# Kernel tuning notes

Measured on AMD Instinct MI355X. Metric: run time of the kernel, lower is better.

## Reference

```python
import jax, jax.numpy as jnp
import numpy as np

SCALE_POS = 2.0
SCALE_NEG = 40.0
THRESH_POS = 0.5
THRESH_NEG = 0.5
MARGIN = 0.1
EPS = 1e-5


def setup_inputs() -> dict:
    key = jax.random.key(0)
    kf, kl = jax.random.split(key)
    B, D, NUM_CLASSES = 4096, 1024, 64
    feats = jax.random.normal(kf, (B, D), dtype=jnp.float32)
    feats = feats / jnp.linalg.norm(feats, axis=1, keepdims=True)  # L2-normalized embeddings
    labels = jax.random.randint(kl, (B,), 0, NUM_CLASSES, dtype=jnp.int64)
    return {"feats": feats, "labels": labels}


def reference(feats, labels):
    B = feats.shape[0]
    sim = jnp.matmul(feats, feats.T)  # [B, B]
    same = labels[:, None] == labels[None, :]
    pos_mask = same & (sim < 1.0 - EPS)  # drop self / near-duplicate pairs
    neg_mask = ~same

    # hard mining: keep negatives above min positive - margin, positives below max negative + margin
    min_pos = jnp.min(jnp.where(pos_mask, sim, jnp.inf), axis=1)   # [B]
    max_neg = jnp.max(jnp.where(neg_mask, sim, -jnp.inf), axis=1)  # [B]
    neg_sel = neg_mask & (sim + MARGIN > min_pos[:, None])
    pos_sel = pos_mask & (sim - MARGIN < max_neg[:, None])

    pos_sum = jnp.sum(jnp.where(pos_sel, jnp.exp(-SCALE_POS * (sim - THRESH_POS)), 0.0), axis=1)
    neg_sum = jnp.sum(jnp.where(neg_sel, jnp.exp(SCALE_NEG * (sim - THRESH_NEG)), 0.0), axis=1)
    pos_loss = jnp.log1p(pos_sum) / SCALE_POS
    neg_loss = jnp.log1p(neg_sum) / SCALE_NEG

    valid = jnp.any(pos_sel, axis=1) & jnp.any(neg_sel, axis=1)  # rows skipped by original loop
    return jnp.sum(jnp.where(valid, pos_loss + neg_loss, 0.0)) / B
```

## Files before the change

kernel.cpp:

```cpp
#include <hip/hip_runtime.h>

typedef float floatx4 __attribute__((ext_vector_type(4)));
typedef int intx4 __attribute__((ext_vector_type(4)));
typedef int intx8 __attribute__((ext_vector_type(8)));
typedef __attribute__((address_space(1))) const void gvoid;
typedef __attribute__((address_space(3))) void svoid;

#define SCALE_POS 2.0f
#define SCALE_NEG 40.0f
#define THRESH 0.5f
#define MARGIN 0.1f
#define EPSV 1e-5f

__global__ void k_init(const float* __restrict__ feats,
                       unsigned char* __restrict__ f8,
                       float* __restrict__ out,
                       int total4) {
    int i = blockIdx.x * blockDim.x + threadIdx.x;
    if (i < total4) {
        float4 v = ((const float4*)feats)[i];
        int w = 0;
        w = __builtin_amdgcn_cvt_pk_fp8_f32(v.x, v.y, w, false);
        w = __builtin_amdgcn_cvt_pk_fp8_f32(v.z, v.w, w, true);
        ((int*)f8)[i] = w;
    }
    if (i == 0) out[0] = 0.f;
}

__global__ void __launch_bounds__(256, 4)
k_gemmA(const unsigned char* __restrict__ f8,
        const int* __restrict__ labels,
        float* __restrict__ pmin,
        float* __restrict__ pmax,
        int D, int nb) {
    __shared__ __align__(16) unsigned char As[128 * 128];
    __shared__ __align__(16) unsigned char Bs[128 * 128];
    __shared__ int labR[128], labC[128];

    const int bid0 = blockIdx.x;
    const int t = (bid0 & 7) * 66 + (bid0 >> 3);
    int rb = 0, rem = t;
    while (rem >= nb - rb) { rem -= nb - rb; ++rb; }
    const int cb = rb + rem;
    const int rowBase = rb * 128;
    const int colBase = cb * 128;

    const int tid = threadIdx.x;
    const int lane = tid & 63;
    const int wave = tid >> 6;
    const int wr = wave >> 1;
    const int wc = wave & 1;
    const int q = lane >> 4;
    const int cIn = lane & 15;

    if (tid < 128) labR[tid] = labels[rowBase + tid];
    else           labC[tid - 128] = labels[colBase + (tid - 128)];

    const int subrow = lane >> 3;
    const int swz = (lane & 7) ^ subrow;
    const unsigned char* gP[8];
    unsigned char* lP[8];
#pragma unroll
    for (int j = 0; j < 8; ++j) {
        const int c = wave * 8 + j;
        const int grow = (c < 16) ? (rowBase + c * 8 + subrow)
                                  : (colBase + (c - 16) * 8 + subrow);
        gP[j] = f8 + (size_t)grow * D + swz * 16;
        lP[j] = ((c < 16) ? (As + c * 1024) : (Bs + (c - 16) * 1024)) + lane * 16;
    }

    int aOff0[4], aOff1[4], bOff0[4], bOff1[4];
#pragma unroll
    for (int i = 0; i < 4; ++i) {
        const int rA = wr * 64 + i * 16 + cIn;
        aOff0[i] = rA * 128 + ((2 * q) ^ (rA & 7)) * 16;
        aOff1[i] = rA * 128 + ((2 * q + 1) ^ (rA & 7)) * 16;
        const int rB = wc * 64 + i * 16 + cIn;
        bOff0[i] = rB * 128 + ((2 * q) ^ (rB & 7)) * 16;
        bOff1[i] = rB * 128 + ((2 * q + 1) ^ (rB & 7)) * 16;
    }

    floatx4 acc[4][4] = {};

    const int KT = D >> 7;
    for (int kt = 0; kt < KT; ++kt) {
        const int kOff = kt * 128;
        __syncthreads();
#pragma unroll
        for (int j = 0; j < 8; ++j)
            __builtin_amdgcn_global_load_lds((gvoid*)(gP[j] + kOff), (svoid*)lP[j], 16, 0, 0);
        __syncthreads();

        intx8 a[4], b[4];
#pragma unroll
        for (int i = 0; i < 4; ++i) {
            intx4 lo = *(const intx4*)(As + aOff0[i]);
            intx4 hi = *(const intx4*)(As + aOff1[i]);
            a[i] = __builtin_shufflevector(lo, hi, 0, 1, 2, 3, 4, 5, 6, 7);
        }
#pragma unroll
        for (int i = 0; i < 4; ++i) {
            intx4 lo = *(const intx4*)(Bs + bOff0[i]);
            intx4 hi = *(const intx4*)(Bs + bOff1[i]);
            b[i] = __builtin_shufflevector(lo, hi, 0, 1, 2, 3, 4, 5, 6, 7);
        }
#pragma unroll
        for (int i = 0; i < 4; ++i)
#pragma unroll
            for (int j2 = 0; j2 < 4; ++j2)
                acc[i][j2] = __builtin_amdgcn_mfma_scale_f32_16x16x128_f8f6f4(
                    a[i], b[j2], acc[i][j2], 0, 0,
                    0, 0x7f7f7f7f, 0, 0x7f7f7f7f);
    }

    int rLabv[16];
#pragma unroll
    for (int mi = 0; mi < 4; ++mi)
#pragma unroll
        for (int rr = 0; rr < 4; ++rr)
            rLabv[mi * 4 + rr] = labR[wr * 64 + mi * 16 + q * 4 + rr];
    int cLabv[4];
#pragma unroll
    for (int ni = 0; ni < 4; ++ni)
        cLabv[ni] = labC[wc * 64 + ni * 16 + cIn];

    {
        const int slotR = 2 * cb + wc;
#pragma unroll
        for (int mi = 0; mi < 4; ++mi)
#pragma unroll
            for (int rr = 0; rr < 4; ++rr) {
                const int rLoc = wr * 64 + mi * 16 + q * 4 + rr;
                const int rLab = rLabv[mi * 4 + rr];
                float vmin = 1e30f, vmax = -1e30f;
#pragma unroll
                for (int ni = 0; ni < 4; ++ni) {
                    float s = acc[mi][ni][rr];
                    if (rLab == cLabv[ni]) {
                        if (s < 1.0f - EPSV) vmin = fminf(vmin, s);
                    } else {
                        vmax = fmaxf(vmax, s);
                    }
                }
#pragma unroll
                for (int off = 8; off; off >>= 1) {
                    vmin = fminf(vmin, __shfl_xor(vmin, off, 16));
                    vmax = fmaxf(vmax, __shfl_xor(vmax, off, 16));
                }
                if (cIn == 0) {
                    pmin[(size_t)(rowBase + rLoc) * 64 + slotR] = vmin;
                    pmax[(size_t)(rowBase + rLoc) * 64 + slotR] = vmax;
                }
            }
    }

    if (rb != cb) {
        const int slotC = 2 * rb + wr;
#pragma unroll
        for (int ni = 0; ni < 4; ++ni) {
            const int cLab = cLabv[ni];
            float vmin = 1e30f, vmax = -1e30f;
#pragma unroll
            for (int mi = 0; mi < 4; ++mi)
#pragma unroll
                for (int rr = 0; rr < 4; ++rr) {
                    float s = acc[mi][ni][rr];
                    if (rLabv[mi * 4 + rr] == cLab) {
                        if (s < 1.0f - EPSV) vmin = fminf(vmin, s);
                    } else {
                        vmax = fmaxf(vmax, s);
                    }
                }
            vmin = fminf(vmin, __shfl_xor(vmin, 16, 64));
            vmin = fminf(vmin, __shfl_xor(vmin, 32, 64));
            vmax = fmaxf(vmax, __shfl_xor(vmax, 16, 64));
            vmax = fmaxf(vmax, __shfl_xor(vmax, 32, 64));
            if (q == 0) {
                const int cLoc = wc * 64 + ni * 16 + cIn;
                pmin[(size_t)(colBase + cLoc) * 64 + slotC] = vmin;
                pmax[(size_t)(colBase + cLoc) * 64 + slotC] = vmax;
            }
        }
    }
}

__global__ void __launch_bounds__(256, 4)
k_gemmB(const unsigned char* __restrict__ f8,
        const int* __restrict__ labels,
        const float* __restrict__ pmin,
        const float* __restrict__ pmax,
        float* __restrict__ psP,
        float* __restrict__ psN,
        int D, int nb) {
    __shared__ __align__(16) unsigned char As[128 * 128];
    __shared__ __align__(16) unsigned char Bs[128 * 128];
    __shared__ int labR[128], labC[128];
    __shared__ float gNR[128], gPR[128], gNC[128], gPC[128];

    const int bid0 = blockIdx.x;
    const int t = (bid0 & 7) * 66 + (bid0 >> 3);
    int rb = 0, rem = t;
    while (rem >= nb - rb) { rem -= nb - rb; ++rb; }
    const int cb = rb + rem;
    const int rowBase = rb * 128;
    const int colBase = cb * 128;

    const int tid = threadIdx.x;
    const int lane = tid & 63;
    const int wave = tid >> 6;
    const int wr = wave >> 1;
    const int wc = wave & 1;
    const int q = lane >> 4;
    const int cIn = lane & 15;

    {
        const int j = tid & 127;
        const int base = (tid < 128) ? (rowBase + j) : (colBase + j);
        const floatx4* pm = (const floatx4*)(pmin + (size_t)base * 64);
        const floatx4* px = (const floatx4*)(pmax + (size_t)base * 64);
        float mn = 1e30f, mx = -1e30f;
#pragma unroll
        for (int k = 0; k < 16; ++k) {
            floatx4 a = pm[k];
            floatx4 b = px[k];
            mn = fminf(mn, fminf(fminf(a[0], a[1]), fminf(a[2], a[3])));
            mx = fmaxf(mx, fmaxf(fmaxf(b[0], b[1]), fmaxf(b[2], b[3])));
        }
        if (tid < 128) {
            labR[j] = labels[rowBase + j];
            gNR[j] = mn - MARGIN;
            gPR[j] = mx + MARGIN;
        } else {
            labC[j] = labels[colBase + j];
            gNC[j] = mn - MARGIN;
            gPC[j] = mx + MARGIN;
        }
    }

    const int subrow = lane >> 3;
    const int swz = (lane & 7) ^ subrow;
    const unsigned char* gP[8];
    unsigned char* lP[8];
#pragma unroll
    for (int j = 0; j < 8; ++j) {
        const int c = wave * 8 + j;
        const int grow = (c < 16) ? (rowBase + c * 8 + subrow)
                                  : (colBase + (c - 16) * 8 + subrow);
        gP[j] = f8 + (size_t)grow * D + swz * 16;
        lP[j] = ((c < 16) ? (As + c * 1024) : (Bs + (c - 16) * 1024)) + lane * 16;
    }

    int aOff0[4], aOff1[4], bOff0[4], bOff1[4];
#pragma unroll
    for (int i = 0; i < 4; ++i) {
        const int rA = wr * 64 + i * 16 + cIn;
        aOff0[i] = rA * 128 + ((2 * q) ^ (rA & 7)) * 16;
        aOff1[i] = rA * 128 + ((2 * q + 1) ^ (rA & 7)) * 16;
        const int rB = wc * 64 + i * 16 + cIn;
        bOff0[i] = rB * 128 + ((2 * q) ^ (rB & 7)) * 16;
        bOff1[i] = rB * 128 + ((2 * q + 1) ^ (rB & 7)) * 16;
    }

    floatx4 acc[4][4] = {};

    const int KT = D >> 7;
    for (int kt = 0; kt < KT; ++kt) {
        const int kOff = kt * 128;
        __syncthreads();
#pragma unroll
        for (int j = 0; j < 8; ++j)
            __builtin_amdgcn_global_load_lds((gvoid*)(gP[j] + kOff), (svoid*)lP[j], 16, 0, 0);
        __syncthreads();

        intx8 a[4], b[4];
#pragma unroll
        for (int i = 0; i < 4; ++i) {
            intx4 lo = *(const intx4*)(As + aOff0[i]);
            intx4 hi = *(const intx4*)(As + aOff1[i]);
            a[i] = __builtin_shufflevector(lo, hi, 0, 1, 2, 3, 4, 5, 6, 7);
        }
#pragma unroll
        for (int i = 0; i < 4; ++i) {
            intx4 lo = *(const intx4*)(Bs + bOff0[i]);
            intx4 hi = *(const intx4*)(Bs + bOff1[i]);
            b[i] = __builtin_shufflevector(lo, hi, 0, 1, 2, 3, 4, 5, 6, 7);
        }
#pragma unroll
        for (int i = 0; i < 4; ++i)
#pragma unroll
            for (int j2 = 0; j2 < 4; ++j2)
                acc[i][j2] = __builtin_amdgcn_mfma_scale_f32_16x16x128_f8f6f4(
                    a[i], b[j2], acc[i][j2], 0, 0,
                    0, 0x7f7f7f7f, 0, 0x7f7f7f7f);
    }

    int rLabv[16];
#pragma unroll
    for (int mi = 0; mi < 4; ++mi)
#pragma unroll
        for (int rr = 0; rr < 4; ++rr)
            rLabv[mi * 4 + rr] = labR[wr * 64 + mi * 16 + q * 4 + rr];
    int cLabv[4];
    float gNCv[4], gPCv[4];
#pragma unroll
    for (int ni = 0; ni < 4; ++ni) {
        const int j = wc * 64 + ni * 16 + cIn;
        cLabv[ni] = labC[j];
        gNCv[ni] = gNC[j];
        gPCv[ni] = gPC[j];
    }

    const bool offd = (rb != cb);
    float cps[4] = {}, cns[4] = {};
    const int slotR = 2 * cb + wc;

#pragma unroll
    for (int mi = 0; mi < 4; ++mi)
#pragma unroll
        for (int rr = 0; rr < 4; ++rr) {
            const int rLoc = wr * 64 + mi * 16 + q * 4 + rr;
            const int rLab = rLabv[mi * 4 + rr];
            const float gn = gNR[rLoc];
            const float gp = gPR[rLoc];
            float rp = 0.f, rn = 0.f;
#pragma unroll
            for (int ni = 0; ni < 4; ++ni) {
                const float s = acc[mi][ni][rr];
                if (rLab == cLabv[ni]) {
                    if (s < 1.0f - EPSV) {
                        float ev = __expf(-SCALE_POS * (s - THRESH));
                        if (s < gp) rp += ev;
                        if (offd && s < gPCv[ni]) cps[ni] += ev;
                    }
                } else {
                    float ev = __expf(SCALE_NEG * (s - THRESH));
                    if (s > gn) rn += ev;
                    if (offd && s > gNCv[ni]) cns[ni] += ev;
                }
            }
#pragma unroll
            for (int off = 8; off; off >>= 1) {
                rp += __shfl_xor(rp, off, 16);
                rn += __shfl_xor(rn, off, 16);
            }
            if (cIn == 0) {
                psP[(size_t)(rowBase + rLoc) * 64 + slotR] = rp;
                psN[(size_t)(rowBase + rLoc) * 64 + slotR] = rn;
            }
        }
    if (offd) {
        const int slotC = 2 * rb + wr;
#pragma unroll
        for (int ni = 0; ni < 4; ++ni) {
            cps[ni] += __shfl_xor(cps[ni], 16, 64);
            cps[ni] += __shfl_xor(cps[ni], 32, 64);
            cns[ni] += __shfl_xor(cns[ni], 16, 64);
            cns[ni] += __shfl_xor(cns[ni], 32, 64);
            if (q == 0) {
                const int cLoc = wc * 64 + ni * 16 + cIn;
                psP[(size_t)(colBase + cLoc) * 64 + slotC] = cps[ni];
                psN[(size_t)(colBase + cLoc) * 64 + slotC] = cns[ni];
            }
        }
    }
}

__global__ void __launch_bounds__(256)
k_final(const float* __restrict__ psP, const float* __restrict__ psN,
        float* __restrict__ out, int B) {
    __shared__ float red[4];
    const int r = blockIdx.x * 256 + threadIdx.x;
    const floatx4* pp = (const floatx4*)(psP + (size_t)r * 64);
    const floatx4* pn = (const floatx4*)(psN + (size_t)r * 64);
    float P = 0.f, N = 0.f;
#pragma unroll
    for (int k = 0; k < 16; ++k) {
        floatx4 a = pp[k];
        P += (a[0] + a[1]) + (a[2] + a[3]);
        floatx4 b = pn[k];
        N += (b[0] + b[1]) + (b[2] + b[3]);
    }
    float a = (P > 0.f && N > 0.f)
                  ? log1pf(P) * (1.0f / SCALE_POS) + log1pf(N) * (1.0f / SCALE_NEG)
                  : 0.f;
#pragma unroll
    for (int off = 32; off; off >>= 1) a += __shfl_down(a, off, 64);
    const int tid = threadIdx.x;
    if ((tid & 63) == 0) red[tid >> 6] = a;
    __syncthreads();
    if (tid == 0)
        atomicAdd(out, (red[0] + red[1] + red[2] + red[3]) / (float)B);
}

extern "C" void kernel_launch(void* const* d_in, const int* in_sizes, int n_in,
                              void* d_out, int out_size, void* d_ws, size_t ws_size,
                              hipStream_t stream) {
    const float* feats = (const float*)d_in[0];
    const int* labels = (const int*)d_in[1];
    const int B = in_sizes[1];
    const int D = in_sizes[0] / B;
    const int nb = B / 128;
    const int NT = nb * (nb + 1) / 2;
    const int total4 = B * D / 4;

    char* ws = (char*)d_ws;
    unsigned char* f8 = (unsigned char*)ws;
    size_t off = (size_t)B * D;
    float* pmin = (float*)(ws + off); off += (size_t)64 * B * 4;
    float* pmax = (float*)(ws + off); off += (size_t)64 * B * 4;
    float* psP  = (float*)(ws + off); off += (size_t)64 * B * 4;
    float* psN  = (float*)(ws + off); off += (size_t)64 * B * 4;
    float* outp = (float*)d_out;

    k_init<<<(total4 + 255) / 256, 256, 0, stream>>>(feats, f8, outp, total4);

    k_gemmA<<<NT, 256, 0, stream>>>(f8, labels, pmin, pmax, D, nb);

    k_gemmB<<<NT, 256, 0, stream>>>(f8, labels, pmin, pmax, psP, psN, D, nb);

    k_final<<<B / 256, 256, 0, stream>>>(psP, psN, outp, B);
}
```

Before: 151.4 us.

## Transpose partial-stat buffers to slot-major and precompute row gates once

Partial min/max and partial sums are now stored slot-major ([slot][row]) rather than row-major with 64 slots per row, so lanes writing consecutive rows produce contiguous stores. A new small k_stats kernel reduces the 64 min/max partials per row once into gate arrays, so each gemmB block no longer re-reads 2x64 floats for all 256 of its rows and columns. The cost is an extra kernel launch, and the final and stats reductions now loop over strided slot rows.

```diff
diff --git a/kernel.cpp b/kernel.cpp
--- a/kernel.cpp
+++ b/kernel.cpp
@@ -37,6 +37,8 @@
     __shared__ __align__(16) unsigned char Bs[128 * 128];
     __shared__ int labR[128], labC[128];
 
+    const int Bsz = nb * 128;
+
     const int bid0 = blockIdx.x;
     const int t = (bid0 & 7) * 66 + (bid0 >> 3);
     int rb = 0, rem = t;
@@ -125,7 +127,8 @@
         cLabv[ni] = labC[wc * 64 + ni * 16 + cIn];
 
     {
-        const int slotR = 2 * cb + wc;
+        float* pmnRow = pmin + (size_t)(2 * cb + wc) * Bsz + rowBase;
+        float* pmxRow = pmax + (size_t)(2 * cb + wc) * Bsz + rowBase;
 #pragma unroll
         for (int mi = 0; mi < 4; ++mi)
 #pragma unroll
@@ -148,14 +151,15 @@
                     vmax = fmaxf(vmax, __shfl_xor(vmax, off, 16));
                 }
                 if (cIn == 0) {
-                    pmin[(size_t)(rowBase + rLoc) * 64 + slotR] = vmin;
-                    pmax[(size_t)(rowBase + rLoc) * 64 + slotR] = vmax;
+                    pmnRow[rLoc] = vmin;
+                    pmxRow[rLoc] = vmax;
                 }
             }
     }
 
     if (rb != cb) {
-        const int slotC = 2 * rb + wr;
+        float* pmnCol = pmin + (size_t)(2 * rb + wr) * Bsz + colBase;
+        float* pmxCol = pmax + (size_t)(2 * rb + wr) * Bsz + colBase;
 #pragma unroll
         for (int ni = 0; ni < 4; ++ni) {
             const int cLab = cLabv[ni];
@@ -177,18 +181,31 @@
             vmax = fmaxf(vmax, __shfl_xor(vmax, 32, 64));
             if (q == 0) {
                 const int cLoc = wc * 64 + ni * 16 + cIn;
-                pmin[(size_t)(colBase + cLoc) * 64 + slotC] = vmin;
-                pmax[(size_t)(colBase + cLoc) * 64 + slotC] = vmax;
-            }
-        }
-    }
+                pmnCol[cLoc] = vmin;
+                pmxCol[cLoc] = vmax;
+            }
+        }
+    }
+}
+
+__global__ void __launch_bounds__(256)
+k_stats(const float* __restrict__ pmin, const float* __restrict__ pmax,
+        float* __restrict__ gateN, float* __restrict__ gateP, int B) {
+    const int r = blockIdx.x * 256 + threadIdx.x;
+    float mn = 1e30f, mx = -1e30f;
+    for (int k = 0; k < 64; ++k) {
+        mn = fminf(mn, pmin[(size_t)k * B + r]);
+        mx = fmaxf(mx, pmax[(size_t)k * B + r]);
+    }
+    gateN[r] = mn - MARGIN;
+    gateP[r] = mx + MARGIN;
 }
 
 __global__ void __launch_bounds__(256, 4)
 k_gemmB(const unsigned char* __restrict__ f8,
         const int* __restrict__ labels,
-        const float* __restrict__ pmin,
-        const float* __restrict__ pmax,
+        const float* __restrict__ gateN,
+        const float* __restrict__ gateP,
         float* __restrict__ psP,
         float* __restrict__ psN,
         int D, int nb) {
@@ -197,6 +214,8 @@
     __shared__ int labR[128], labC[128];
     __shared__ float gNR[128], gPR[128], gNC[128], gPC[128];
 
+    const int Bsz = nb * 128;
+
     const int bid0 = blockIdx.x;
     const int t = (bid0 & 7) * 66 + (bid0 >> 3);
     int rb = 0, rem = t;
@@ -213,28 +232,15 @@
     const int q = lane >> 4;
     const int cIn = lane & 15;
 
-    {
-        const int j = tid & 127;
-        const int base = (tid < 128) ? (rowBase + j) : (colBase + j);
-        const floatx4* pm = (const floatx4*)(pmin + (size_t)base * 64);
-        const floatx4* px = (const floatx4*)(pmax + (size_t)base * 64);
-        float mn = 1e30f, mx = -1e30f;
-#pragma unroll
-        for (int k = 0; k < 16; ++k) {
-            floatx4 a = pm[k];
-            floatx4 b = px[k];
-            mn = fminf(mn, fminf(fminf(a[0], a[1]), fminf(a[2], a[3])));
-            mx = fmaxf(mx, fmaxf(fmaxf(b[0], b[1]), fmaxf(b[2], b[3])));
-        }
-        if (tid < 128) {
-            labR[j] = labels[rowBase + j];
-            gNR[j] = mn - MARGIN;
-            gPR[j] = mx + MARGIN;
-        } else {
-            labC[j] = labels[colBase + j];
-            gNC[j] = mn - MARGIN;
-            gPC[j] = mx + MARGIN;
-        }
+    if (tid < 128) {
+        labR[tid] = labels[rowBase + tid];
+        gNR[tid] = gateN[rowBase + tid];
+        gPR[tid] = gateP[rowBase + tid];
+    } else {
+        const int j = tid - 128;
+        labC[j] = labels[colBase + j];
+        gNC[j] = gateN[colBase + j];
+        gPC[j] = gateP[colBase + j];
     }
 
     const int subrow = lane >> 3;
@@ -312,7 +318,8 @@
 
     const bool offd = (rb != cb);
     float cps[4] = {}, cns[4] = {};
-    const int slotR = 2 * cb + wc;
+    float* psPRow = psP + (size_t)(2 * cb + wc) * Bsz + rowBase;
+    float* psNRow = psN + (size_t)(2 * cb + wc) * Bsz + rowBase;
 
 #pragma unroll
     for (int mi = 0; mi < 4; ++mi)
@@ -344,12 +351,13 @@
                 rn += __shfl_xor(rn, off, 16);
             }
             if (cIn == 0) {
-                psP[(size_t)(rowBase + rLoc) * 64 + slotR] = rp;
-                psN[(size_t)(rowBase + rLoc) * 64 + slotR] = rn;
+                psPRow[rLoc] = rp;
+                psNRow[rLoc] = rn;
             }
         }
     if (offd) {
-        const int slotC = 2 * rb + wr;
+        float* psPCol = psP + (size_t)(2 * rb + wr) * Bsz + colBase;
+        float* psNCol = psN + (size_t)(2 * rb + wr) * Bsz + colBase;
 #pragma unroll
         for (int ni = 0; ni < 4; ++ni) {
             cps[ni] += __shfl_xor(cps[ni], 16, 64);
@@ -358,8 +366,8 @@
             cns[ni] += __shfl_xor(cns[ni], 32, 64);
             if (q == 0) {
                 const int cLoc = wc * 64 + ni * 16 + cIn;
-                psP[(size_t)(colBase + cLoc) * 64 + slotC] = cps[ni];
-                psN[(size_t)(colBase + cLoc) * 64 + slotC] = cns[ni];
+                psPCol[cLoc] = cps[ni];
+                psNCol[cLoc] = cns[ni];
             }
         }
     }
@@ -370,15 +378,10 @@
         float* __restrict__ out, int B) {
     __shared__ float red[4];
     const int r = blockIdx.x * 256 + threadIdx.x;
-    const floatx4* pp = (const floatx4*)(psP + (size_t)r * 64);
-    const floatx4* pn = (const floatx4*)(psN + (size_t)r * 64);
     float P = 0.f, N = 0.f;
-#pragma unroll
-    for (int k = 0; k < 16; ++k) {
-        floatx4 a = pp[k];
-        P += (a[0] + a[1]) + (a[2] + a[3]);
-        floatx4 b = pn[k];
-        N += (b[0] + b[1]) + (b[2] + b[3]);
+    for (int k = 0; k < 64; ++k) {
+        P += psP[(size_t)k * B + r];
+        N += psN[(size_t)k * B + r];
     }
     float a = (P > 0.f && N > 0.f)
                   ? log1pf(P) * (1.0f / SCALE_POS) + log1pf(N) * (1.0f / SCALE_NEG)
@@ -410,13 +413,17 @@
     float* pmax = (float*)(ws + off); off += (size_t)64 * B * 4;
     float* psP  = (float*)(ws + off); off += (size_t)64 * B * 4;
     float* psN  = (float*)(ws + off); off += (size_t)64 * B * 4;
+    float* gateN = (float*)(ws + off); off += (size_t)B * 4;
+    float* gateP = (float*)(ws + off); off += (size_t)B * 4;
     float* outp = (float*)d_out;
 
     k_init<<<(total4 + 255) / 256, 256, 0, stream>>>(feats, f8, outp, total4);
 
     k_gemmA<<<NT, 256, 0, stream>>>(f8, labels, pmin, pmax, D, nb);
 
-    k_gemmB<<<NT, 256, 0, stream>>>(f8, labels, pmin, pmax, psP, psN, D, nb);
+    k_stats<<<B / 256, 256, 0, stream>>>(pmin, pmax, gateN, gateP, B);
+
+    k_gemmB<<<NT, 256, 0, stream>>>(f8, labels, gateN, gateP, psP, psN, D, nb);
 
     k_final<<<B / 256, 256, 0, stream>>>(psP, psN, outp, B);
 }
```

Result: slower. 155.8 us (+2.9%).
